# Kernel tuning notes

Measured on AMD Instinct MI355X. Metric: run time of the kernel, lower is better.

## Reference

```python
import jax, jax.numpy as jnp
import numpy as np

# ---- fixed problem dimensions ----
B, S, T = 64, 200, 32          # batch of sequences, trees per seq, nodes per tree
V, E, C = 50000, 128, 128      # vocab, embedding_dim, encode_dim
H, OUT = 100, 104              # GRU hidden, output_dim
N = B * S * T                  # total nodes
D_MAX = 5                      # max depth of a 32-node complete binary tree


def setup_inputs() -> dict:
    key = jax.random.key(0)
    ks = jax.random.split(key, 16)
    # --- tree structure: every tree is a complete binary tree with T nodes ---
    local_parent = np.array([0] + [(i - 1) // 2 for i in range(1, T)], dtype=np.int64)
    local_depth = np.array([int(np.floor(np.log2(i + 1))) for i in range(T)], dtype=np.int64)
    num_trees = B * S
    offsets = np.arange(num_trees, dtype=np.int64) * T
    node_parent = (offsets[:, None] + local_parent[None, :]).reshape(-1)
    node_depth = np.tile(local_depth, num_trees)
    node_tree = np.repeat(np.arange(num_trees, dtype=np.int64), T)
    node_tokens = jax.random.randint(ks[0], (N,), 0, V, dtype=jnp.int64)
    sc = 0.05
    inp = {
        "node_tokens": node_tokens,
        "node_parent": jnp.asarray(node_parent),
        "node_tree": jnp.asarray(node_tree),
        "node_depth": jnp.asarray(node_depth),
        "emb": jax.random.normal(ks[1], (V, E), jnp.float32) * sc,
        "w_lin": jax.random.normal(ks[2], (C, E), jnp.float32) * sc,
        "b_lin": jnp.zeros((C,), jnp.float32),
        "w_ih_f": jax.random.normal(ks[3], (3 * H, C), jnp.float32) * sc,
        "w_hh_f": jax.random.normal(ks[4], (3 * H, H), jnp.float32) * sc,
        "b_ih_f": jnp.zeros((3 * H,), jnp.float32),
        "b_hh_f": jnp.zeros((3 * H,), jnp.float32),
        "w_ih_b": jax.random.normal(ks[5], (3 * H, C), jnp.float32) * sc,
        "w_hh_b": jax.random.normal(ks[6], (3 * H, H), jnp.float32) * sc,
        "b_ih_b": jnp.zeros((3 * H,), jnp.float32),
        "b_hh_b": jnp.zeros((3 * H,), jnp.float32),
        "fc_w": jax.random.normal(ks[7], (OUT, 2 * H), jnp.float32) * sc,
        "fc_b": jnp.zeros((OUT,), jnp.float32),
    }
    return inp


def _gru(x_sbc, w_ih, w_hh, b_ih, b_hh):
    """Torch-convention GRU over leading time axis. x_sbc: [S, B, C] -> [S, B, H]."""
    h0 = jnp.zeros((x_sbc.shape[1], w_hh.shape[1]), x_sbc.dtype)

    def step(h, xt):
        gx = xt @ w_ih.T + b_ih
        gh = h @ w_hh.T + b_hh
        xr, xz, xn = jnp.split(gx, 3, axis=-1)
        hr, hz, hn = jnp.split(gh, 3, axis=-1)
        r = jax.nn.sigmoid(xr + hr)
        z = jax.nn.sigmoid(xz + hz)
        n = jnp.tanh(xn + r * hn)
        h_new = (1.0 - z) * n + z * h
        return h_new, h_new

    _, hs = jax.lax.scan(step, h0, x_sbc)
    return hs


def reference(node_tokens, node_parent, node_tree, node_depth,
              emb, w_lin, b_lin,
              w_ih_f, w_hh_f, b_ih_f, b_hh_f,
              w_ih_b, w_hh_b, b_ih_b, b_hh_b,
              fc_w, fc_b):
    # per-node contribution: W * emb(token) + b   (recursion base of hidden_state)
    c = emb[node_tokens] @ w_lin.T + b_lin               # [N, C]
    # level-batched bottom-up scatter-add: h(node) = c(node) + sum(h(children))
    h = c
    for d in range(D_MAX, 0, -1):
        mask = (node_depth == d)[:, None]
        h = h.at[node_parent].add(jnp.where(mask, h, 0.0))
    # per-tree max pool over all node hidden states (TreeEncoder output)
    tree_vec = jax.ops.segment_max(h, node_tree, num_segments=B * S)  # [B*S, C]
    x = tree_vec.reshape(B, S, C)
    # bidirectional GRU (batch_first in torch; scan over time here)
    x_t = jnp.transpose(x, (1, 0, 2))                    # [S, B, C]
    fwd = _gru(x_t, w_ih_f, w_hh_f, b_ih_f, b_hh_f)      # [S, B, H]
    bwd = _gru(x_t[::-1], w_ih_b, w_hh_b, b_ih_b, b_hh_b)[::-1]
    gru_out = jnp.concatenate([fwd, bwd], axis=-1)       # [S, B, 2H]
    pool = gru_out.max(axis=0)                           # [B, 2H] (max over time)
    return pool @ fc_w.T + fc_b                          # [B, OUT]
```

## Files before the change

kernel.cpp:

```cpp
#include <hip/hip_runtime.h>
#include <hip/hip_bf16.h>
#include <math.h>

#define BB 64
#define SS 200
#define TT 32
#define VV 50000
#define EE 128
#define CC 128
#define HH 100
#define G3 300
#define OUTD 104
#define NTREE (BB*SS)

typedef __attribute__((ext_vector_type(4))) float f32x4;
typedef _Float16 f16x8 __attribute__((ext_vector_type(8)));

__device__ inline float fast_sigmoid(float x) {
    return __builtin_amdgcn_rcpf(1.f + __builtin_amdgcn_exp2f(-1.4426950408889634f * x));
}
__device__ inline float fast_tanh(float x) {
    return 1.f - 2.f * __builtin_amdgcn_rcpf(1.f + __builtin_amdgcn_exp2f(2.8853900817779268f * x));
}

#define BAR() asm volatile("s_waitcnt lgkmcnt(0)\n\ts_barrier" ::: "memory")


__global__ __launch_bounds__(256) void k0_prep(const float* __restrict__ w_lin,
                                               const float* __restrict__ w_ih_f,
                                               const float* __restrict__ w_ih_b,
                                               const float* __restrict__ emb,
                                               _Float16* __restrict__ wl,
                                               _Float16* __restrict__ k2b,
                                               _Float16* __restrict__ emb16) {
    const int tid  = threadIdx.x;
    const int wave = tid >> 6;
    const int lane = tid & 63;
    const int r = lane & 15;
    const int q = lane >> 4;
    if (blockIdx.x == 0) {
#pragma unroll
        for (int nt = 0; nt < 2; ++nt)
#pragma unroll
            for (int kt = 0; kt < 4; ++kt) {
                const int n = wave * 32 + nt * 16 + r;
                const float* src = w_lin + (long)n * EE + kt * 32 + q * 8;
                f16x8 f;
#pragma unroll
                for (int e = 0; e < 8; ++e) f[e] = (_Float16)src[e];
                *(f16x8*)&wl[(size_t)((((wave * 2 + nt) * 4 + kt) * 64) + lane) * 8] = f;
            }
    } else if (blockIdx.x <= 10) {
        const int nb = blockIdx.x - 1;
        const int n = nb * 64 + wave * 16 + r;
        const int dir = (n >= 320) ? 1 : 0;
        const int j = n - dir * 320;
        const int jj = (j < G3) ? j : 0;
        const float* w = dir ? w_ih_b : w_ih_f;
#pragma unroll
        for (int kt = 0; kt < 4; ++kt) {
            const float* src = w + (long)jj * EE + kt * 32 + q * 8;
            f16x8 f;
#pragma unroll
            for (int e = 0; e < 8; ++e) f[e] = (_Float16)src[e];
            *(f16x8*)&k2b[(size_t)((((nb * 4 + wave) * 4 + kt) * 64) + lane) * 8] = f;
        }
    } else {
        const long base = (long)(blockIdx.x - 11) * 2048 + (long)tid * 8;
        if (base < (long)VV * EE) {
            const float4* s = (const float4*)(emb + base);
            const float4 v0 = s[0], v1 = s[1];
            f16x8 f;
            f[0] = (_Float16)v0.x; f[1] = (_Float16)v0.y;
            f[2] = (_Float16)v0.z; f[3] = (_Float16)v0.w;
            f[4] = (_Float16)v1.x; f[5] = (_Float16)v1.y;
            f[6] = (_Float16)v1.z; f[7] = (_Float16)v1.w;
            *(f16x8*)&emb16[base] = f;
        }
    }
}

#define K1_TPI 2
#define AROWS (K1_TPI*TT)
#define LDA 136
#define LDC 132

__global__ __launch_bounds__(256) void k1_mfma(const int* __restrict__ tok,
                                               const _Float16* __restrict__ emb16,
                                               const _Float16* __restrict__ wl,
                                               const float* __restrict__ b_lin,
                                               _Float16* __restrict__ thi) {
    __shared__ __align__(16) _Float16 A_sh[AROWS * LDA];
    __shared__ __align__(16) float C_sh[AROWS * LDC];
    __shared__ int tok_sh[AROWS];

    const int tid  = threadIdx.x;
    const int wave = tid >> 6;
    const int lane = tid & 63;
    const int r = lane & 15;
    const int q = lane >> 4;

    f16x8 bfrag[2][4];
    float bias[2];
#pragma unroll
    for (int nt = 0; nt < 2; ++nt) {
        bias[nt] = b_lin[wave * 32 + nt * 16 + r];
#pragma unroll
        for (int kt = 0; kt < 4; ++kt)
            bfrag[nt][kt] = *(const f16x8*)&wl[(size_t)((((wave * 2 + nt) * 4 + kt) * 64) + lane) * 8];
    }

    const int tree0 = blockIdx.x * K1_TPI;
    if (tid < AROWS) tok_sh[tid] = tok[tree0 * TT + tid];
    __syncthreads();

#pragma unroll
    for (int i = 0; i < 4; ++i) {
        const int idx = tid + i * 256;
        const int row = idx >> 4;
        const int p   = idx & 15;
        const f16x8 v = *(const f16x8*)&emb16[(long)tok_sh[row] * EE + p * 8];
        *(f16x8*)&A_sh[row * LDA + p * 8] = v;
    }
    __syncthreads();

    f32x4 acc[4][2];
#pragma unroll
    for (int mt = 0; mt < 4; ++mt)
#pragma unroll
        for (int nt = 0; nt < 2; ++nt) acc[mt][nt] = (f32x4)(0.f);

#pragma unroll
    for (int mt = 0; mt < 4; ++mt) {
        const int m = mt * 16 + r;
        f16x8 afrag[4];
#pragma unroll
        for (int kt = 0; kt < 4; ++kt)
            afrag[kt] = *(const f16x8*)&A_sh[m * LDA + kt * 32 + q * 8];
#pragma unroll
        for (int nt = 0; nt < 2; ++nt)
#pragma unroll
            for (int kt = 0; kt < 4; ++kt)
                acc[mt][nt] = __builtin_amdgcn_mfma_f32_16x16x32_f16(
                    afrag[kt], bfrag[nt][kt], acc[mt][nt], 0, 0, 0);
    }

#pragma unroll
    for (int mt = 0; mt < 4; ++mt)
#pragma unroll
        for (int nt = 0; nt < 2; ++nt) {
            const int col = wave * 32 + nt * 16 + r;
#pragma unroll
            for (int reg = 0; reg < 4; ++reg) {
                const int row = mt * 16 + q * 4 + reg;
                C_sh[row * LDC + col] = acc[mt][nt][reg] + bias[nt];
            }
        }
    __syncthreads();

    {
        const int t = tid >> 7;
        const int j = tid & 127;
        const float* base = &C_sh[(t * TT) * LDC + j];
        float v[TT];
#pragma unroll
        for (int n = 0; n < TT; ++n) v[n] = base[n * LDC];
        float mx = -1e30f;
#pragma unroll
        for (int n = TT - 1; n >= 1; --n) {
            mx = fmaxf(mx, v[n]);
            v[(n - 1) >> 1] += v[n];
        }
        mx = fmaxf(mx, v[0]);
        thi[(size_t)(tree0 + t) * CC + j] = (_Float16)mx;
    }
}

__global__ __launch_bounds__(256) void k2_mfma(const _Float16* __restrict__ thi,
                                               const _Float16* __restrict__ k2b,
                                               const float* __restrict__ b_ih_f,
                                               const float* __restrict__ b_ih_b,
                                               float* __restrict__ gx) {
    __shared__ __align__(16) _Float16 Ah[32 * LDA];

    const int tid  = threadIdx.x;
    const int wave = tid >> 6;
    const int lane = tid & 63;
    const int r = lane & 15;
    const int q = lane >> 4;

    const int nb = blockIdx.x % 10;
    const int mb = blockIdx.x / 10;
    const int m0 = mb * 32;
    const int n0 = nb * 64;

#pragma unroll
    for (int i = 0; i < 2; ++i) {
        const int idx = tid + i * 256;
        const int row = idx >> 4;
        const int p   = idx & 15;
        f16x8 v = *(const f16x8*)&thi[(size_t)(m0 + row) * CC + p * 8];
        *(f16x8*)&Ah[row * LDA + p * 8] = v;
    }
    f16x8 bh[4];
#pragma unroll
    for (int kt = 0; kt < 4; ++kt)
        bh[kt] = *(const f16x8*)&k2b[(size_t)((((nb * 4 + wave) * 4 + kt) * 64) + lane) * 8];
    __syncthreads();

    f32x4 acc[2];
    acc[0] = (f32x4)(0.f); acc[1] = (f32x4)(0.f);
#pragma unroll
    for (int mt = 0; mt < 2; ++mt) {
        const int m = mt * 16 + r;
#pragma unroll
        for (int kt = 0; kt < 4; ++kt) {
            f16x8 a = *(const f16x8*)&Ah[m * LDA + kt * 32 + q * 8];
            acc[mt] = __builtin_amdgcn_mfma_f32_16x16x32_f16(a, bh[kt], acc[mt], 0, 0, 0);
        }
    }

    const int ng  = n0 + wave * 16 + r;
    const int dir = (ng >= 320) ? 1 : 0;
    const int j   = ng - dir * 320;
    const bool valid = (j < G3);
    const float bias = valid ? (dir ? b_ih_b[j] : b_ih_f[j]) : 0.f;
    float* gxd = gx + (long)dir * NTREE * G3;
    if (valid) {
#pragma unroll
        for (int mt = 0; mt < 2; ++mt)
#pragma unroll
            for (int reg = 0; reg < 4; ++reg) {
                const int m = m0 + mt * 16 + q * 4 + reg;
                gxd[(long)m * G3 + j] = acc[mt][reg] + bias;
            }
    }
}

__global__ __launch_bounds__(512, 2) void k3_gru(const float* __restrict__ gx,
                                                 const float* __restrict__ w_hh_f,
                                                 const float* __restrict__ b_hh_f,
                                                 const float* __restrict__ w_hh_b,
                                                 const float* __restrict__ b_hh_b,
                                                 float* __restrict__ pool) {
    const int b    = blockIdx.x;
    const int tid  = threadIdx.x;
    const int dir  = tid >> 8;
    const int wave = (tid >> 6) & 3;
    const int lane = tid & 63;
    const int r = lane & 15;
    const int q = lane >> 4;

    const float* w_hh = dir ? w_hh_b : w_hh_f;
    const float* b_hh = dir ? b_hh_b : b_hh_f;

    __shared__ __align__(16) _Float16 h_sh[2][2][128];

    f16x8 bf[6][4];
#pragma unroll
    for (int i = 0; i < 6; ++i) {
        const int gate = (i < 3) ? i : i - 3;
        const int ch   = (i < 3) ? r : 16 + r;
        const bool nv  = (ch < 25);
        const int row  = gate * HH + wave * 25 + (nv ? ch : 0);
#pragma unroll
        for (int kt = 0; kt < 4; ++kt) {
            f16x8 f;
#pragma unroll
            for (int e = 0; e < 8; ++e) {
                const int k = kt * 32 + q * 8 + e;
                f[e] = (_Float16)((nv && k < HH) ? w_hh[row * HH + k] : 0.f);
            }
            bf[i][kt] = f;
        }
    }

    const int m = lane;
    const int c = wave * 25 + m;
    const bool act  = (m < 25);
    const bool lo16 = (m < 16);
    float br = 0.f, bz = 0.f, bn = 0.f;
    if (act) { br = b_hh[c]; bz = b_hh[HH + c]; bn = b_hh[2 * HH + c]; }

    if ((tid & 255) < 128) {
        h_sh[dir][0][tid & 127] = (_Float16)0.f;
        h_sh[dir][1][tid & 127] = (_Float16)0.f;
    }

    const int sstep = dir ? -1 : 1;
    const int s0 = dir ? (SS - 1) : 0;
    const float* gp = gx + (long)dir * NTREE * G3 + (long)b * SS * G3 + c;

    float pxr[4], pxz[4], pxn[4];
    if (act) {
#pragma unroll
        for (int j = 0; j < 4; ++j) {
            const long off = (long)(s0 + j * sstep) * G3;
            pxr[j] = gp[off]; pxz[j] = gp[off + HH]; pxn[j] = gp[off + 2 * HH];
        }
    }
    float hj = 0.f, hmax = -1e30f;
    __syncthreads();

    int s = s0;
    for (int t = 0; t < SS; t += 4) {
#pragma unroll
        for (int j = 0; j < 4; ++j) {
            const int p = j & 1;

            f16x8 a[4];
#pragma unroll
            for (int kt = 0; kt < 4; ++kt)
                a[kt] = *(const f16x8*)&h_sh[dir][p][kt * 32 + q * 8];

            f32x4 accA[6], accB[6];
#pragma unroll
            for (int i = 0; i < 6; ++i) {
                accA[i] = (f32x4)(0.f);
                accB[i] = (f32x4)(0.f);
                accA[i] = __builtin_amdgcn_mfma_f32_16x16x32_f16(a[0], bf[i][0], accA[i], 0, 0, 0);
                accB[i] = __builtin_amdgcn_mfma_f32_16x16x32_f16(a[2], bf[i][2], accB[i], 0, 0, 0);
                accA[i] = __builtin_amdgcn_mfma_f32_16x16x32_f16(a[1], bf[i][1], accA[i], 0, 0, 0);
                accB[i] = __builtin_amdgcn_mfma_f32_16x16x32_f16(a[3], bf[i][3], accB[i], 0, 0, 0);
            }
            const float G0 = accA[0][0] + accB[0][0];
            const float G1 = accA[1][0] + accB[1][0];
            const float G2 = accA[2][0] + accB[2][0];
            const float G3v = accA[3][0] + accB[3][0];
            const float G4 = accA[4][0] + accB[4][0];
            const float G5 = accA[5][0] + accB[5][0];
            const float ghr = lo16 ? G0 : G3v;
            const float ghz = lo16 ? G1 : G4;
            const float ghn = lo16 ? G2 : G5;

            if (act) {
                const float rg = fast_sigmoid(pxr[j] + ghr + br);
                const float zg = fast_sigmoid(pxz[j] + ghz + bz);
                const float ng = fast_tanh(pxn[j] + rg * (ghn + bn));
                hj = (1.f - zg) * ng + zg * hj;
                h_sh[dir][1 - p][c] = (_Float16)hj;
                hmax = fmaxf(hmax, hj);
                if (t + j + 4 < SS) {
                    const long off = (long)(s + (j + 4) * sstep) * G3;
                    pxr[j] = gp[off]; pxz[j] = gp[off + HH]; pxn[j] = gp[off + 2 * HH];
                }
            }
            BAR();
        }
        s += 4 * sstep;
    }
    if (act) pool[(long)b * (2 * HH) + dir * HH + c] = hmax;
}

__global__ __launch_bounds__(256) void k4_fc(const float* __restrict__ pool,
                                             const float* __restrict__ fc_w,
                                             const float* __restrict__ fc_b,
                                             float* __restrict__ out) {
    const int b = blockIdx.x;
    __shared__ __align__(16) float p_sh[2 * HH];
    const int t = threadIdx.x;
    if (t < 2 * HH) p_sh[t] = pool[(long)b * (2 * HH) + t];
    __syncthreads();
    if (t < OUTD) {
        const float4* wr4 = (const float4*)(fc_w + (long)t * (2 * HH));
        const float4* p4 = (const float4*)p_sh;
        float a0 = 0.f, a1 = 0.f;
#pragma unroll
        for (int k = 0; k < 50; k += 2) {
            float4 w0 = wr4[k],   p0 = p4[k];
            float4 w1 = wr4[k+1], p1 = p4[k+1];
            a0 += w0.x*p0.x + w0.y*p0.y + w0.z*p0.z + w0.w*p0.w;
            a1 += w1.x*p1.x + w1.y*p1.y + w1.z*p1.z + w1.w*p1.w;
        }
        out[(long)b * OUTD + t] = fc_b[t] + a0 + a1;
    }
}

extern "C" void kernel_launch(void* const* d_in, const int* in_sizes, int n_in,
                              void* d_out, int out_size, void* d_ws, size_t ws_size,
                              hipStream_t stream) {
    const int*   tok    = (const int*)d_in[0];
    const float* emb    = (const float*)d_in[4];
    const float* w_lin  = (const float*)d_in[5];
    const float* b_lin  = (const float*)d_in[6];
    const float* w_ih_f = (const float*)d_in[7];
    const float* w_hh_f = (const float*)d_in[8];
    const float* b_ih_f = (const float*)d_in[9];
    const float* b_hh_f = (const float*)d_in[10];
    const float* w_ih_b = (const float*)d_in[11];
    const float* w_hh_b = (const float*)d_in[12];
    const float* b_ih_b = (const float*)d_in[13];
    const float* b_hh_b = (const float*)d_in[14];
    const float* fc_w   = (const float*)d_in[15];
    const float* fc_b   = (const float*)d_in[16];

    char* wsb = (char*)d_ws;
    _Float16* wl    = (_Float16*)(wsb);
    _Float16* k2b   = (_Float16*)(wsb + 32768);
    _Float16* thi   = (_Float16*)(wsb + 196608);
    float*    gx    = (float*)(wsb + 3473408);
    _Float16* emb16 = (_Float16*)(wsb + 3473408);
    float*    pool  = (float*)(wsb);
    float*    out   = (float*)d_out;

    k0_prep<<<11 + 3125, 256, 0, stream>>>(w_lin, w_ih_f, w_ih_b, emb, wl, k2b, emb16);
    k1_mfma<<<NTREE / K1_TPI, 256, 0, stream>>>(tok, emb16, wl, b_lin, thi);
    k2_mfma<<<(NTREE / 32) * 10, 256, 0, stream>>>(thi, k2b, b_ih_f, b_ih_b, gx);
    k3_gru <<<BB, 512, 0, stream>>>(gx, w_hh_f, b_hh_f, w_hh_b, b_hh_b, pool);
    k4_fc  <<<BB, 256, 0, stream>>>(pool, fc_w, fc_b, out);
}
```

Baseline: 264.6 us.

## Split GRU per direction into separate 2-wave blocks with prepacked fp16 recurrent weights

The GRU kernel now launches one 128-thread block per (batch, direction) instead of one 512-thread block covering both directions. Each of the two waves owns 50 hidden channels and issues 48 MFMAs per step rather than 24 across four waves, so each barrier spans fewer waves. The recurrent weights are converted and packed into MFMA fragment layout once in the prep kernel, which replaces the strided per-block fp32 loads. In exchange, the MFMA work on the serial critical path per wave roughly doubles, and register pressure rises from holding 48 weight fragments plus 12 accumulators.

Measured after the change: 287.6 us. 8.7% more time.

```diff
diff --git a/kernel.cpp b/kernel.cpp
--- a/kernel.cpp
+++ b/kernel.cpp
@@ -29,9 +29,12 @@
 __global__ __launch_bounds__(256) void k0_prep(const float* __restrict__ w_lin,
                                                const float* __restrict__ w_ih_f,
                                                const float* __restrict__ w_ih_b,
+                                               const float* __restrict__ w_hh_f,
+                                               const float* __restrict__ w_hh_b,
                                                const float* __restrict__ emb,
                                                _Float16* __restrict__ wl,
                                                _Float16* __restrict__ k2b,
+                                               _Float16* __restrict__ k3b,
                                                _Float16* __restrict__ emb16) {
     const int tid  = threadIdx.x;
     const int wave = tid >> 6;
@@ -65,8 +68,32 @@
             for (int e = 0; e < 8; ++e) f[e] = (_Float16)src[e];
             *(f16x8*)&k2b[(size_t)((((nb * 4 + wave) * 4 + kt) * 64) + lane) * 8] = f;
         }
+    } else if (blockIdx.x <= 14) {
+        const int dw = blockIdx.x - 11;
+        const int d  = dw >> 1;
+        const int wh = dw & 1;
+        const float* whh = d ? w_hh_b : w_hh_f;
+#pragma unroll
+        for (int tt = 0; tt < 3; ++tt) {
+            const int t = wave * 3 + tt;
+            const int g  = t % 3;
+            const int cb = t / 3;
+            const int cc = cb * 16 + r;
+            const bool nv = (cc < 50);
+            const int row = g * HH + 50 * wh + (nv ? cc : 0);
+#pragma unroll
+            for (int kt = 0; kt < 4; ++kt) {
+                f16x8 f;
+#pragma unroll
+                for (int e = 0; e < 8; ++e) {
+                    const int k = kt * 32 + q * 8 + e;
+                    f[e] = (_Float16)((nv && k < HH) ? whh[row * HH + k] : 0.f);
+                }
+                *(f16x8*)&k3b[(size_t)((((dw * 12 + t) * 4 + kt) * 64) + lane) * 8] = f;
+            }
+        }
     } else {
-        const long base = (long)(blockIdx.x - 11) * 2048 + (long)tid * 8;
+        const long base = (long)(blockIdx.x - 15) * 2048 + (long)tid * 8;
         if (base < (long)VV * EE) {
             const float4* s = (const float4*)(emb + base);
             const float4 v0 = s[0], v1 = s[1];
@@ -237,55 +264,40 @@
     }
 }
 
-__global__ __launch_bounds__(512, 2) void k3_gru(const float* __restrict__ gx,
-                                                 const float* __restrict__ w_hh_f,
+__global__ __launch_bounds__(128, 1) void k3_gru(const float* __restrict__ gx,
+                                                 const _Float16* __restrict__ k3b,
                                                  const float* __restrict__ b_hh_f,
-                                                 const float* __restrict__ w_hh_b,
                                                  const float* __restrict__ b_hh_b,
                                                  float* __restrict__ pool) {
-    const int b    = blockIdx.x;
-    const int tid  = threadIdx.x;
-    const int dir  = tid >> 8;
-    const int wave = (tid >> 6) & 3;
+    const int bid = blockIdx.x;
+    const int dir = bid & 1;
+    const int b   = bid >> 1;
+    const int tid = threadIdx.x;
+    const int wh   = tid >> 6;
     const int lane = tid & 63;
     const int r = lane & 15;
     const int q = lane >> 4;
 
-    const float* w_hh = dir ? w_hh_b : w_hh_f;
     const float* b_hh = dir ? b_hh_b : b_hh_f;
 
-    __shared__ __align__(16) _Float16 h_sh[2][2][128];
-
-    f16x8 bf[6][4];
-#pragma unroll
-    for (int i = 0; i < 6; ++i) {
-        const int gate = (i < 3) ? i : i - 3;
-        const int ch   = (i < 3) ? r : 16 + r;
-        const bool nv  = (ch < 25);
-        const int row  = gate * HH + wave * 25 + (nv ? ch : 0);
-#pragma unroll
-        for (int kt = 0; kt < 4; ++kt) {
-            f16x8 f;
-#pragma unroll
-            for (int e = 0; e < 8; ++e) {
-                const int k = kt * 32 + q * 8 + e;
-                f[e] = (_Float16)((nv && k < HH) ? w_hh[row * HH + k] : 0.f);
-            }
-            bf[i][kt] = f;
-        }
-    }
-
-    const int m = lane;
-    const int c = wave * 25 + m;
-    const bool act  = (m < 25);
-    const bool lo16 = (m < 16);
+    __shared__ __align__(16) _Float16 h_sh[2][128];
+
+    const int dw = dir * 2 + wh;
+    f16x8 bf[12][4];
+#pragma unroll
+    for (int t = 0; t < 12; ++t)
+#pragma unroll
+        for (int kt = 0; kt < 4; ++kt)
+            bf[t][kt] = *(const f16x8*)&k3b[(size_t)((((dw * 12 + t) * 4 + kt) * 64) + lane) * 8];
+
+    const int cc = q * 16 + r;
+    const bool act = (cc < 50);
+    const int c = 50 * wh + cc;
     float br = 0.f, bz = 0.f, bn = 0.f;
     if (act) { br = b_hh[c]; bz = b_hh[HH + c]; bn = b_hh[2 * HH + c]; }
 
-    if ((tid & 255) < 128) {
-        h_sh[dir][0][tid & 127] = (_Float16)0.f;
-        h_sh[dir][1][tid & 127] = (_Float16)0.f;
-    }
+    h_sh[0][tid] = (_Float16)0.f;
+    h_sh[1][tid] = (_Float16)0.f;
 
     const int sstep = dir ? -1 : 1;
     const int s0 = dir ? (SS - 1) : 0;
@@ -303,7 +315,7 @@
     __syncthreads();
 
     int s = s0;
-    for (int t = 0; t < SS; t += 4) {
+    for (int t0 = 0; t0 < SS; t0 += 4) {
 #pragma unroll
         for (int j = 0; j < 4; ++j) {
             const int p = j & 1;
@@ -311,36 +323,28 @@
             f16x8 a[4];
 #pragma unroll
             for (int kt = 0; kt < 4; ++kt)
-                a[kt] = *(const f16x8*)&h_sh[dir][p][kt * 32 + q * 8];
-
-            f32x4 accA[6], accB[6];
-#pragma unroll
-            for (int i = 0; i < 6; ++i) {
-                accA[i] = (f32x4)(0.f);
-                accB[i] = (f32x4)(0.f);
-                accA[i] = __builtin_amdgcn_mfma_f32_16x16x32_f16(a[0], bf[i][0], accA[i], 0, 0, 0);
-                accB[i] = __builtin_amdgcn_mfma_f32_16x16x32_f16(a[2], bf[i][2], accB[i], 0, 0, 0);
-                accA[i] = __builtin_amdgcn_mfma_f32_16x16x32_f16(a[1], bf[i][1], accA[i], 0, 0, 0);
-                accB[i] = __builtin_amdgcn_mfma_f32_16x16x32_f16(a[3], bf[i][3], accB[i], 0, 0, 0);
-            }
-            const float G0 = accA[0][0] + accB[0][0];
-            const float G1 = accA[1][0] + accB[1][0];
-            const float G2 = accA[2][0] + accB[2][0];
-            const float G3v = accA[3][0] + accB[3][0];
-            const float G4 = accA[4][0] + accB[4][0];
-            const float G5 = accA[5][0] + accB[5][0];
-            const float ghr = lo16 ? G0 : G3v;
-            const float ghz = lo16 ? G1 : G4;
-            const float ghn = lo16 ? G2 : G5;
+                a[kt] = *(const f16x8*)&h_sh[p][kt * 32 + q * 8];
+
+            f32x4 acc[12];
+#pragma unroll
+            for (int i = 0; i < 12; ++i) {
+                acc[i] = (f32x4)(0.f);
+#pragma unroll
+                for (int kt = 0; kt < 4; ++kt)
+                    acc[i] = __builtin_amdgcn_mfma_f32_16x16x32_f16(a[kt], bf[i][kt], acc[i], 0, 0, 0);
+            }
+            const float ghr = (q == 0) ? acc[0][0] : (q == 1) ? acc[3][0] : (q == 2) ? acc[6][0] : acc[9][0];
+            const float ghz = (q == 0) ? acc[1][0] : (q == 1) ? acc[4][0] : (q == 2) ? acc[7][0] : acc[10][0];
+            const float ghn = (q == 0) ? acc[2][0] : (q == 1) ? acc[5][0] : (q == 2) ? acc[8][0] : acc[11][0];
 
             if (act) {
                 const float rg = fast_sigmoid(pxr[j] + ghr + br);
                 const float zg = fast_sigmoid(pxz[j] + ghz + bz);
                 const float ng = fast_tanh(pxn[j] + rg * (ghn + bn));
                 hj = (1.f - zg) * ng + zg * hj;
-                h_sh[dir][1 - p][c] = (_Float16)hj;
+                h_sh[1 - p][c] = (_Float16)hj;
                 hmax = fmaxf(hmax, hj);
-                if (t + j + 4 < SS) {
+                if (t0 + j + 4 < SS) {
                     const long off = (long)(s + (j + 4) * sstep) * G3;
                     pxr[j] = gp[off]; pxz[j] = gp[off + HH]; pxn[j] = gp[off + 2 * HH];
                 }
@@ -398,14 +402,16 @@
     _Float16* wl    = (_Float16*)(wsb);
     _Float16* k2b   = (_Float16*)(wsb + 32768);
     _Float16* thi   = (_Float16*)(wsb + 196608);
-    float*    gx    = (float*)(wsb + 3473408);
-    _Float16* emb16 = (_Float16*)(wsb + 3473408);
+    _Float16* k3b   = (_Float16*)(wsb + 3473408);
+    float*    gx    = (float*)(wsb + 3670016);
+    _Float16* emb16 = (_Float16*)(wsb + 3670016);
     float*    pool  = (float*)(wsb);
     float*    out   = (float*)d_out;
 
-    k0_prep<<<11 + 3125, 256, 0, stream>>>(w_lin, w_ih_f, w_ih_b, emb, wl, k2b, emb16);
+    k0_prep<<<15 + 3125, 256, 0, stream>>>(w_lin, w_ih_f, w_ih_b, w_hh_f, w_hh_b, emb,
+                                           wl, k2b, k3b, emb16);
     k1_mfma<<<NTREE / K1_TPI, 256, 0, stream>>>(tok, emb16, wl, b_lin, thi);
     k2_mfma<<<(NTREE / 32) * 10, 256, 0, stream>>>(thi, k2b, b_ih_f, b_ih_b, gx);
-    k3_gru <<<BB, 512, 0, stream>>>(gx, w_hh_f, b_hh_f, w_hh_b, b_hh_b, pool);
+    k3_gru <<<2 * BB, 128, 0, stream>>>(gx, k3b, b_hh_f, b_hh_b, pool);
     k4_fc  <<<BB, 256, 0, stream>>>(pool, fc_w, fc_b, out);
 }
```

## Split GRU directions into separate blocks and prescale recurrent weights in prep

Applied to the files above, without the earlier changes.

The GRU kernel now launches one 256-thread block per (batch, direction) instead of one 512-thread block per batch. Each block synchronizes only its own four waves and uses a private h buffer, so barriers cover fewer waves and twice as many blocks can spread across CUs. The recurrent weights are converted to fp16 and prescaled by log2(e) factors once in the prep kernel and loaded as packed fragments. This removes per-element conversion in the GRU prologue and folds the exp2 scaling and biases into FMAs. Prescaling before the fp16 conversion slightly changes rounding.

After: 292.6 us. 1.11x slower.

```diff
diff --git a/kernel.cpp b/kernel.cpp
--- a/kernel.cpp
+++ b/kernel.cpp
@@ -16,12 +16,9 @@
 typedef __attribute__((ext_vector_type(4))) float f32x4;
 typedef _Float16 f16x8 __attribute__((ext_vector_type(8)));
 
-__device__ inline float fast_sigmoid(float x) {
-    return __builtin_amdgcn_rcpf(1.f + __builtin_amdgcn_exp2f(-1.4426950408889634f * x));
-}
-__device__ inline float fast_tanh(float x) {
-    return 1.f - 2.f * __builtin_amdgcn_rcpf(1.f + __builtin_amdgcn_exp2f(2.8853900817779268f * x));
-}
+#define L2E  1.4426950408889634f
+#define NL2E (-1.4426950408889634f)
+#define TL2E 2.8853900817779268f
 
 #define BAR() asm volatile("s_waitcnt lgkmcnt(0)\n\ts_barrier" ::: "memory")
 
@@ -29,9 +26,12 @@
 __global__ __launch_bounds__(256) void k0_prep(const float* __restrict__ w_lin,
                                                const float* __restrict__ w_ih_f,
                                                const float* __restrict__ w_ih_b,
+                                               const float* __restrict__ w_hh_f,
+                                               const float* __restrict__ w_hh_b,
                                                const float* __restrict__ emb,
                                                _Float16* __restrict__ wl,
                                                _Float16* __restrict__ k2b,
+                                               _Float16* __restrict__ k3b,
                                                _Float16* __restrict__ emb16) {
     const int tid  = threadIdx.x;
     const int wave = tid >> 6;
@@ -65,8 +65,29 @@
             for (int e = 0; e < 8; ++e) f[e] = (_Float16)src[e];
             *(f16x8*)&k2b[(size_t)((((nb * 4 + wave) * 4 + kt) * 64) + lane) * 8] = f;
         }
+    } else if (blockIdx.x <= 12) {
+        const int d = blockIdx.x - 11;
+        const float* whh = d ? w_hh_b : w_hh_f;
+#pragma unroll
+        for (int t = 0; t < 6; ++t) {
+            const int gate = (t < 3) ? t : t - 3;
+            const int ch   = (t < 3) ? r : 16 + r;
+            const bool nv  = (ch < 25);
+            const int row  = gate * HH + wave * 25 + (nv ? ch : 0);
+            const float sc = (gate == 2) ? TL2E : NL2E;
+#pragma unroll
+            for (int kt = 0; kt < 4; ++kt) {
+                f16x8 f;
+#pragma unroll
+                for (int e = 0; e < 8; ++e) {
+                    const int k = kt * 32 + q * 8 + e;
+                    f[e] = (_Float16)((nv && k < HH) ? sc * whh[row * HH + k] : 0.f);
+                }
+                *(f16x8*)&k3b[(size_t)((((d * 4 + wave) * 6 + t) * 4 + kt) * 64 + lane) * 8] = f;
+            }
+        }
     } else {
-        const long base = (long)(blockIdx.x - 11) * 2048 + (long)tid * 8;
+        const long base = (long)(blockIdx.x - 13) * 2048 + (long)tid * 8;
         if (base < (long)VV * EE) {
             const float4* s = (const float4*)(emb + base);
             const float4 v0 = s[0], v1 = s[1];
@@ -237,55 +258,44 @@
     }
 }
 
-__global__ __launch_bounds__(512, 2) void k3_gru(const float* __restrict__ gx,
-                                                 const float* __restrict__ w_hh_f,
+__global__ __launch_bounds__(256, 1) void k3_gru(const float* __restrict__ gx,
+                                                 const _Float16* __restrict__ k3b,
                                                  const float* __restrict__ b_hh_f,
-                                                 const float* __restrict__ w_hh_b,
                                                  const float* __restrict__ b_hh_b,
                                                  float* __restrict__ pool) {
-    const int b    = blockIdx.x;
-    const int tid  = threadIdx.x;
-    const int dir  = tid >> 8;
-    const int wave = (tid >> 6) & 3;
+    const int bid = blockIdx.x;
+    const int dir = bid & 1;
+    const int b   = bid >> 1;
+    const int tid = threadIdx.x;
+    const int wave = tid >> 6;
     const int lane = tid & 63;
     const int r = lane & 15;
     const int q = lane >> 4;
 
-    const float* w_hh = dir ? w_hh_b : w_hh_f;
     const float* b_hh = dir ? b_hh_b : b_hh_f;
 
-    __shared__ __align__(16) _Float16 h_sh[2][2][128];
-
+    __shared__ __align__(16) _Float16 h_sh[2][128];
+
+    const int dw = dir * 4 + wave;
     f16x8 bf[6][4];
 #pragma unroll
-    for (int i = 0; i < 6; ++i) {
-        const int gate = (i < 3) ? i : i - 3;
-        const int ch   = (i < 3) ? r : 16 + r;
-        const bool nv  = (ch < 25);
-        const int row  = gate * HH + wave * 25 + (nv ? ch : 0);
-#pragma unroll
-        for (int kt = 0; kt < 4; ++kt) {
-            f16x8 f;
-#pragma unroll
-            for (int e = 0; e < 8; ++e) {
-                const int k = kt * 32 + q * 8 + e;
-                f[e] = (_Float16)((nv && k < HH) ? w_hh[row * HH + k] : 0.f);
-            }
-            bf[i][kt] = f;
-        }
-    }
+    for (int t = 0; t < 6; ++t)
+#pragma unroll
+        for (int kt = 0; kt < 4; ++kt)
+            bf[t][kt] = *(const f16x8*)&k3b[(size_t)(((dw * 6 + t) * 4 + kt) * 64 + lane) * 8];
 
     const int m = lane;
     const int c = wave * 25 + m;
     const bool act  = (m < 25);
     const bool lo16 = (m < 16);
-    float br = 0.f, bz = 0.f, bn = 0.f;
-    if (act) { br = b_hh[c]; bz = b_hh[HH + c]; bn = b_hh[2 * HH + c]; }
-
-    if ((tid & 255) < 128) {
-        h_sh[dir][0][tid & 127] = (_Float16)0.f;
-        h_sh[dir][1][tid & 127] = (_Float16)0.f;
-    }
+    float brc = 0.f, bzc = 0.f, bnc = 0.f;
+    if (act) {
+        brc = NL2E * b_hh[c];
+        bzc = NL2E * b_hh[HH + c];
+        bnc = TL2E * b_hh[2 * HH + c];
+    }
+
+    if (tid < 128) { h_sh[0][tid] = (_Float16)0.f; h_sh[1][tid] = (_Float16)0.f; }
 
     const int sstep = dir ? -1 : 1;
     const int s0 = dir ? (SS - 1) : 0;
@@ -296,14 +306,16 @@
 #pragma unroll
         for (int j = 0; j < 4; ++j) {
             const long off = (long)(s0 + j * sstep) * G3;
-            pxr[j] = gp[off]; pxz[j] = gp[off + HH]; pxn[j] = gp[off + 2 * HH];
+            pxr[j] = __builtin_fmaf(gp[off], NL2E, brc);
+            pxz[j] = __builtin_fmaf(gp[off + HH], NL2E, bzc);
+            pxn[j] = gp[off + 2 * HH] * TL2E;
         }
     }
     float hj = 0.f, hmax = -1e30f;
     __syncthreads();
 
     int s = s0;
-    for (int t = 0; t < SS; t += 4) {
+    for (int t0 = 0; t0 < SS; t0 += 4) {
 #pragma unroll
         for (int j = 0; j < 4; ++j) {
             const int p = j & 1;
@@ -311,7 +323,7 @@
             f16x8 a[4];
 #pragma unroll
             for (int kt = 0; kt < 4; ++kt)
-                a[kt] = *(const f16x8*)&h_sh[dir][p][kt * 32 + q * 8];
+                a[kt] = *(const f16x8*)&h_sh[p][kt * 32 + q * 8];
 
             f32x4 accA[6], accB[6];
 #pragma unroll
@@ -334,15 +346,20 @@
             const float ghn = lo16 ? G2 : G5;
 
             if (act) {
-                const float rg = fast_sigmoid(pxr[j] + ghr + br);
-                const float zg = fast_sigmoid(pxz[j] + ghz + bz);
-                const float ng = fast_tanh(pxn[j] + rg * (ghn + bn));
-                hj = (1.f - zg) * ng + zg * hj;
-                h_sh[dir][1 - p][c] = (_Float16)hj;
+                const float rg = __builtin_amdgcn_rcpf(1.f + __builtin_amdgcn_exp2f(pxr[j] + ghr));
+                const float zg = __builtin_amdgcn_rcpf(1.f + __builtin_amdgcn_exp2f(pxz[j] + ghz));
+                const float t1 = ghn + bnc;
+                const float an = __builtin_fmaf(rg, t1, pxn[j]);
+                const float u  = __builtin_amdgcn_rcpf(1.f + __builtin_amdgcn_exp2f(an));
+                const float n  = __builtin_fmaf(-2.f, u, 1.f);
+                hj = __builtin_fmaf(zg, hj - n, n);
+                h_sh[1 - p][c] = (_Float16)hj;
                 hmax = fmaxf(hmax, hj);
-                if (t + j + 4 < SS) {
+                if (t0 + j + 4 < SS) {
                     const long off = (long)(s + (j + 4) * sstep) * G3;
-                    pxr[j] = gp[off]; pxz[j] = gp[off + HH]; pxn[j] = gp[off + 2 * HH];
+                    pxr[j] = __builtin_fmaf(gp[off], NL2E, brc);
+                    pxz[j] = __builtin_fmaf(gp[off + HH], NL2E, bzc);
+                    pxn[j] = gp[off + 2 * HH] * TL2E;
                 }
             }
             BAR();
@@ -398,14 +415,16 @@
     _Float16* wl    = (_Float16*)(wsb);
     _Float16* k2b   = (_Float16*)(wsb + 32768);
     _Float16* thi   = (_Float16*)(wsb + 196608);
-    float*    gx    = (float*)(wsb + 3473408);
-    _Float16* emb16 = (_Float16*)(wsb + 3473408);
+    _Float16* k3b   = (_Float16*)(wsb + 3473408);
+    float*    gx    = (float*)(wsb + 3670016);
+    _Float16* emb16 = (_Float16*)(wsb + 3670016);
     float*    pool  = (float*)(wsb);
     float*    out   = (float*)d_out;
 
-    k0_prep<<<11 + 3125, 256, 0, stream>>>(w_lin, w_ih_f, w_ih_b, emb, wl, k2b, emb16);
+    k0_prep<<<13 + 3125, 256, 0, stream>>>(w_lin, w_ih_f, w_ih_b, w_hh_f, w_hh_b, emb,
+                                           wl, k2b, k3b, emb16);
     k1_mfma<<<NTREE / K1_TPI, 256, 0, stream>>>(tok, emb16, wl, b_lin, thi);
     k2_mfma<<<(NTREE / 32) * 10, 256, 0, stream>>>(thi, k2b, b_ih_f, b_ih_b, gx);
-    k3_gru <<<BB, 512, 0, stream>>>(gx, w_hh_f, b_hh_f, w_hh_b, b_hh_b, pool);
+    k3_gru <<<2 * BB, 256, 0, stream>>>(gx, k3b, b_hh_f, b_hh_b, pool);
     k4_fc  <<<BB, 256, 0, stream>>>(pool, fc_w, fc_b, out);
 }
```
